# Performance work log

Hardware: AMD Instinct MI355X
Metric: run time of the kernel (lower is better)

## Reference

```python
import jax, jax.numpy as jnp
import numpy as np

B, N, D = 4, 4096, 512      # batch, seq_len, model width
DIM_K = 64                   # per-head key dim used ONLY for the 1/sqrt scale
PROJ = 512                   # dim_k*heads = dim_v*heads = 64*8


def setup_inputs() -> dict:
    key = jax.random.key(0)
    ks = jax.random.split(key, 11)
    glorot = lambda k, shape: jax.random.uniform(
        k, shape, jnp.float32,
        -np.sqrt(6.0 / (shape[0] + shape[1])), np.sqrt(6.0 / (shape[0] + shape[1])))
    return {
        "q": jax.random.normal(ks[0], (B, N, D), jnp.float32),
        "k": jax.random.normal(ks[1], (B, N, D), jnp.float32),
        "v": jax.random.normal(ks[2], (B, N, D), jnp.float32),
        "w_q": glorot(ks[3], (D, PROJ)),
        "w_k": glorot(ks[4], (D, PROJ)),
        "w_v": glorot(ks[5], (D, PROJ)),
        "w_mha": glorot(ks[6], (PROJ, D)),
        "b_q": jnp.zeros((1, 1, PROJ), jnp.float32),
        "b_k": jnp.zeros((1, 1, PROJ), jnp.float32),
        "b_v": jnp.zeros((1, 1, PROJ), jnp.float32),
        "b_mha": jnp.zeros((1, 1, D), jnp.float32),
    }


def reference(q, k, v, w_q, w_k, w_v, w_mha, b_q, b_k, b_v, b_mha):
    # Projections (tensordot over last axis + broadcast bias)
    qp = jnp.einsum('bnd,de->bne', q, w_q) + b_q
    kp = jnp.einsum('bnd,de->bne', k, w_k) + b_k
    vp = jnp.einsum('bnd,de->bne', v, w_v) + b_v
    # NOTE: original call() forgets to pass heads=self.heads, so heads=1:
    # a single attention over the full PROJ width, scaled by sqrt(DIM_K).
    atts = jnp.einsum('bqe,bke->bqk', qp, kp) / np.sqrt(DIM_K).astype(np.float32)
    atts = jax.nn.softmax(atts, axis=-1)      # [B, N, N]
    dpa = jnp.einsum('bqk,bke->bqe', atts, vp)
    return jnp.einsum('bne,ed->bnd', dpa, w_mha) + b_mha
```

## Files before the change

### kernel.cpp

```cpp
#include <hip/hip_runtime.h>
#include <hip/hip_bf16.h>


typedef __attribute__((ext_vector_type(8))) short bf16x8;
typedef __attribute__((ext_vector_type(4))) float f32x4;

#define NB 4
#define NN 4096
#define ND 512

__device__ __forceinline__ f32x4 mfma16(bf16x8 a, bf16x8 b, f32x4 c) {
    return __builtin_amdgcn_mfma_f32_16x16x32_bf16(a, b, c, 0, 0, 0);
}
__device__ __forceinline__ short f2bf(float f) {
    __hip_bfloat16 h = __float2bfloat16(f);
    return *reinterpret_cast<short*>(&h);
}

typedef __attribute__((address_space(1))) const unsigned int gls_gt;
typedef __attribute__((address_space(3))) unsigned int gls_lt;
__device__ __forceinline__ void gll16(const void* g, void* l) {
    __builtin_amdgcn_global_load_lds((gls_gt*)g, (gls_lt*)l, 16, 0, 0);
}

#define DPP_ROR_STEP(V, CTRL, OP)                                              \
    {                                                                          \
        int _t = __builtin_amdgcn_update_dpp(0, __float_as_int(V), (CTRL),     \
                                             0xf, 0xf, true);                  \
        (V) = OP((V), __int_as_float(_t));                                     \
    }
__device__ __forceinline__ float faddf(float a, float b) { return a + b; }
__device__ __forceinline__ float rmax16(float v) {
    DPP_ROR_STEP(v, 0x128, fmaxf)
    DPP_ROR_STEP(v, 0x124, fmaxf)
    DPP_ROR_STEP(v, 0x122, fmaxf)
    DPP_ROR_STEP(v, 0x121, fmaxf)
    return v;
}
__device__ __forceinline__ float rsum16(float v) {
    DPP_ROR_STEP(v, 0x128, faddf)
    DPP_ROR_STEP(v, 0x124, faddf)
    DPP_ROR_STEP(v, 0x122, faddf)
    DPP_ROR_STEP(v, 0x121, faddf)
    return v;
}

struct Ptrs4 {
    const float* in[4];
    short* out[4];
};

__global__ void transpose_w(Ptrs4 p) {
    __shared__ short tile[32][33];
    const float* in = p.in[blockIdx.z];
    short* out = p.out[blockIdx.z];
    int r0 = blockIdx.y * 32, c0 = blockIdx.x * 32;
    int tx = threadIdx.x, ty = threadIdx.y;
    for (int i = 0; i < 32; i += 8)
        tile[ty + i][tx] = f2bf(in[(r0 + ty + i) * 512 + c0 + tx]);
    __syncthreads();
    for (int i = 0; i < 32; i += 8)
        out[(c0 + ty + i) * 512 + r0 + tx] = tile[tx][ty + i];
}

template <int AF32, int VT, int OF32>
__global__ __launch_bounds__(256, 2) void gemm_bt_bias(
    const void* __restrict__ Av, const short* __restrict__ Bt,
    const float* __restrict__ bias, void* __restrict__ C) {
    __shared__ __align__(1024) char As[2][16384];
    __shared__ __align__(1024) char Bs[2][16384];
    int tid = threadIdx.x;
    int lane = tid & 63, w = tid >> 6;
    int l15 = lane & 15, l4 = lane >> 4;
    int wr2 = (w & 1) * 64, wc2 = (w >> 1) * 64;
    int m0 = blockIdx.x * 128, n0 = blockIdx.y * 128;
    f32x4 acc[16] = {};

    int sr = lane >> 3;
    int sd = ((lane & 7) ^ sr) << 3;

#define STAGE_B(BUF, KT)                                                    \
    {                                                                       \
        _Pragma("unroll")                                                   \
        for (int i = 0; i < 4; i++) {                                       \
            int rbase = i * 32 + w * 8;                                     \
            gll16(&Bt[(size_t)(n0 + rbase + sr) * 512 + (KT) + sd],         \
                  Bs[BUF] + rbase * 128);                                   \
        }                                                                   \
    }
#define STAGE_A16(BUF, KT)                                                  \
    {                                                                       \
        const short* A16 = (const short*)Av;                                \
        _Pragma("unroll")                                                   \
        for (int i = 0; i < 4; i++) {                                       \
            int rbase = i * 32 + w * 8;                                     \
            gll16(&A16[(size_t)(m0 + rbase + sr) * 512 + (KT) + sd],        \
                  As[BUF] + rbase * 128);                                   \
        }                                                                   \
    }

    float4 areg[8];
    int arow = w * 32 + (lane >> 4);
    int akc = lane & 15;
#define LOAD_A32(KT)                                                        \
    {                                                                       \
        const float* A32 = (const float*)Av;                                \
        _Pragma("unroll")                                                   \
        for (int inst = 0; inst < 8; inst++)                                \
            areg[inst] = ((const float4*)(A32 +                             \
                (size_t)(m0 + arow + inst * 4) * 512 + (KT)))[akc];         \
    }
#define WRITE_A32(BUF)                                                      \
    {                                                                       \
        _Pragma("unroll")                                                   \
        for (int inst = 0; inst < 8; inst++) {                              \
            int r = arow + inst * 4;                                        \
            short pk[4];                                                    \
            pk[0] = f2bf(areg[inst].x); pk[1] = f2bf(areg[inst].y);         \
            pk[2] = f2bf(areg[inst].z); pk[3] = f2bf(areg[inst].w);         \
            *(long long*)(As[BUF] + r * 128 +                               \
                (((akc >> 1) ^ (r & 7)) << 4) + ((akc & 1) << 3)) =         \
                *(const long long*)pk;                                      \
        }                                                                   \
    }

    if (AF32) {
        LOAD_A32(0);
        STAGE_B(0, 0);
        WRITE_A32(0);
    } else {
        STAGE_A16(0, 0);
        STAGE_B(0, 0);
    }
    for (int t = 0; t < 8; t++) {
        __syncthreads();
        if (t < 7) {
            if (AF32) {
                LOAD_A32((t + 1) * 64);
            } else {
                STAGE_A16((t + 1) & 1, (t + 1) * 64);
            }
            STAGE_B((t + 1) & 1, (t + 1) * 64);
        }
        const char* Ab = As[t & 1];
        const char* Bb = Bs[t & 1];
#pragma unroll
        for (int kb = 0; kb < 2; kb++) {
            int ph = ((((kb << 2) | l4) ^ (l15 & 7)) << 4);
            bf16x8 af[4], bfr[4];
#pragma unroll
            for (int mi = 0; mi < 4; mi++)
                af[mi] = *(const bf16x8*)(Ab + (wr2 + mi * 16 + l15) * 128 + ph);
#pragma unroll
            for (int ni = 0; ni < 4; ni++)
                bfr[ni] = *(const bf16x8*)(Bb + (wc2 + ni * 16 + l15) * 128 + ph);
#pragma unroll
            for (int mi = 0; mi < 4; mi++)
#pragma unroll
                for (int ni = 0; ni < 4; ni++)
                    acc[mi * 4 + ni] = mfma16(af[mi], bfr[ni], acc[mi * 4 + ni]);
        }
        if (AF32 && t < 7) WRITE_A32((t + 1) & 1);
    }
#undef STAGE_B
#undef STAGE_A16
#undef LOAD_A32
#undef WRITE_A32
    if (OF32) {
        for (int mi = 0; mi < 4; mi++)
            for (int ni = 0; ni < 4; ni++) {
                f32x4 vv = acc[mi * 4 + ni];
                int col = n0 + wc2 + ni * 16 + l15;
                float bv = bias[col];
                for (int r = 0; r < 4; r++) {
                    int row = m0 + wr2 + mi * 16 + l4 * 4 + r;
                    ((float*)C)[(size_t)row * 512 + col] = vv[r] + bv;
                }
            }
    } else if (VT) {
        __syncthreads();
        short* Ct = (short*)As;
#pragma unroll
        for (int mi = 0; mi < 4; mi++)
#pragma unroll
            for (int ni = 0; ni < 4; ni++) {
                f32x4 vv = acc[mi * 4 + ni];
                int col = wc2 + ni * 16 + l15;
                float bv = bias[n0 + col];
                int r0w = wr2 + mi * 16 + l4 * 4;
                short pk[4];
#pragma unroll
                for (int r = 0; r < 4; r++) pk[r] = f2bf(vv[r] + bv);
                int byteoff = col * 256 + ((r0w * 2) ^ ((col & 7) << 4));
                *(long long*)((char*)Ct + byteoff) = *(const long long*)pk;
            }
        __syncthreads();
        int b = m0 >> 12;
        short* Cb = (short*)C + (size_t)b * (ND * NN) + (m0 & 4095);
#pragma unroll
        for (int s = 0; s < 8; s++) {
            int col = (tid >> 4) + 16 * s;
            int j = tid & 15;
            int byteoff = col * 256 + ((16 * j) ^ ((col & 7) << 4));
            bf16x8 vvv = *(const bf16x8*)((char*)Ct + byteoff);
            *(bf16x8*)(Cb + (size_t)(n0 + col) * NN + 8 * j) = vvv;
        }
    } else {
        __syncthreads();
        short* Ct = (short*)As;
#pragma unroll
        for (int mi = 0; mi < 4; mi++)
#pragma unroll
            for (int ni = 0; ni < 4; ni++) {
                f32x4 vv = acc[mi * 4 + ni];
                int col = wc2 + ni * 16 + l15;
                float bv = bias[n0 + col];
#pragma unroll
                for (int r = 0; r < 4; r++) {
                    int row = wr2 + mi * 16 + l4 * 4 + r;
                    int byteoff = row * 256 + ((col * 2) ^ ((row & 3) << 5));
                    *(short*)((char*)Ct + byteoff) = f2bf(vv[r] + bv);
                }
            }
        __syncthreads();
#pragma unroll
        for (int s = 0; s < 8; s++) {
            int row = (tid >> 4) + 16 * s;
            int j = tid & 15;
            int byteoff = row * 256 + ((16 * j) ^ ((row & 3) << 5));
            bf16x8 vvv = *(const bf16x8*)((char*)Ct + byteoff);
            *(bf16x8*)((short*)C + (size_t)(m0 + row) * 512 + n0 + 8 * j) = vvv;
        }
    }
}

__global__ __launch_bounds__(512, 2) void flash_attn(
    const short* __restrict__ qp, const short* __restrict__ kp,
    const short* __restrict__ vpT, short* __restrict__ dpa) {
    __shared__ __align__(1024) char KsB[65536];
    __shared__ __align__(1024) char VsB[65536];
    __shared__ __align__(16)   char PldB[8192];
    __shared__ float SexM[128];
    __shared__ float SexS[128];

    int tid = threadIdx.x;
    int lane = tid & 63, w = tid >> 6;
    int l15 = lane & 15, l4 = lane >> 4;
    int wr = w & 3;
    int wc = w >> 2;
    int b = blockIdx.y;
    int q0 = blockIdx.x * 64;

    const short* qpb = qp + b * (NN * ND);
    const short* kpb = kp + b * (NN * ND);
    const short* vtb = vpT + b * (ND * NN);

    bf16x8 qf[16];
    {
        const short* qrow = qpb + (q0 + wr * 16 + l15) * ND + l4 * 8;
#pragma unroll
        for (int kb = 0; kb < 16; kb++) qf[kb] = *(const bf16x8*)(qrow + kb * 32);
    }
    f32x4 oacc[16] = {};
    float m_run[4], l_run[4];
#pragma unroll
    for (int r = 0; r < 4; r++) { m_run[r] = -1e30f; l_run[r] = 0.f; }

    const int vsl0 = ((l4 ^ (l15 & 7)) << 4);
    const int vsl1 = vsl0 ^ 64;

#define STAGE_K(J0)                                                         \
    {                                                                       \
        _Pragma("unroll")                                                   \
        for (int c = 0; c < 8; c++) {                                       \
            int key = w * 8 + c;                                            \
            const short* src = kpb + (size_t)((J0) + key) * ND +            \
                               ((lane ^ (key & 15)) << 3);                  \
            gll16(src, KsB + key * 1024);                                   \
        }                                                                   \
    }
#define STAGE_V(J0)                                                         \
    {                                                                       \
        _Pragma("unroll")                                                   \
        for (int c = 0; c < 8; c++) {                                       \
            int g = w * 8 + c;                                              \
            int e = g * 8 + (lane >> 3);                                    \
            const short* src = vtb + (size_t)e * NN + (J0) +                \
                               (((lane & 7) ^ (e & 7)) << 3);               \
            gll16(src, VsB + g * 1024);                                     \
        }                                                                   \
    }

    STAGE_K(0);
    STAGE_V(0);
    __syncthreads();

    for (int j0 = 0; j0 < NN; j0 += 64) {
        f32x4 s0 = {}, s1 = {};
        {
            const char* kb0 = KsB + (32 * wc + l15) * 1024;
            const char* kb1 = kb0 + 16 * 1024;
#pragma unroll
            for (int kb = 0; kb < 16; kb++) {
                int sl = ((((kb << 2) | l4) ^ l15) << 4);
                s0 = mfma16(qf[kb], *(const bf16x8*)(kb0 + sl), s0);
                s1 = mfma16(qf[kb], *(const bf16x8*)(kb1 + sl), s1);
            }
        }
        float vv0[4], vv1[4], mx[4], ss[4], p0[4], p1[4];
#pragma unroll
        for (int r = 0; r < 4; r++) {
            vv0[r] = s0[r] * 0.125f;
            vv1[r] = s1[r] * 0.125f;
            mx[r] = rmax16(fmaxf(vv0[r], vv1[r]));
        }
#pragma unroll
        for (int r = 0; r < 4; r++) {
            p0[r] = __expf(vv0[r] - mx[r]);
            p1[r] = __expf(vv1[r] - mx[r]);
            ss[r] = rsum16(p0[r] + p1[r]);
        }
        int row4 = wr * 16 + l4 * 4;
        if (l15 == 0) {
#pragma unroll
            for (int r = 0; r < 4; r++) {
                SexM[wc * 64 + row4 + r] = mx[r];
                SexS[wc * 64 + row4 + r] = ss[r];
            }
        }
        __syncthreads();
        float al4[4];
#pragma unroll
        for (int r = 0; r < 4; r++) {
            int row = row4 + r;
            float mo = SexM[(wc ^ 1) * 64 + row];
            float so = SexS[(wc ^ 1) * 64 + row];
            float mt = fmaxf(mx[r], mo);
            float st = ss[r] * __expf(mx[r] - mt) + so * __expf(mo - mt);
            float mn = fmaxf(m_run[r], mt);
            float al = __expf(m_run[r] - mn);
            l_run[r] = l_run[r] * al + st * __expf(mt - mn);
            m_run[r] = mn;
            al4[r] = al;
            float fs = __expf(mx[r] - mn);
            int rw7 = row & 7;
            char* prow = PldB + row * 128;
            int col0 = wc * 32 + l15;
            *(short*)(prow + (((col0 >> 3) ^ rw7) << 4) + ((col0 & 7) << 1)) = f2bf(p0[r] * fs);
            int col1 = col0 + 16;
            *(short*)(prow + (((col1 >> 3) ^ rw7) << 4) + ((col1 & 7) << 1)) = f2bf(p1[r] * fs);
        }
        {
            bool need = (al4[0] != 1.f) | (al4[1] != 1.f) |
                        (al4[2] != 1.f) | (al4[3] != 1.f);
            if (__any(need)) {
#pragma unroll
                for (int t = 0; t < 16; t++)
#pragma unroll
                    for (int r = 0; r < 4; r++) oacc[t][r] *= al4[r];
            }
        }
        __syncthreads();
        if (j0 + 64 < NN) STAGE_K(j0 + 64);
        bf16x8 pa0, pa1;
        {
            const char* prow = PldB + (wr * 16 + l15) * 128;
            pa0 = *(const bf16x8*)(prow + vsl0);
            pa1 = *(const bf16x8*)(prow + vsl1);
        }
#pragma unroll
        for (int eh = 0; eh < 2; eh++) {
#pragma unroll
            for (int i = 0; i < 8; i++) {
                const char* vb = VsB + (eh * 256 + 32 * i + 16 * wc + l15) * 128;
                int oi = eh * 8 + i;
                oacc[oi] = mfma16(pa0, *(const bf16x8*)(vb + vsl0), oacc[oi]);
                oacc[oi] = mfma16(pa1, *(const bf16x8*)(vb + vsl1), oacc[oi]);
            }
        }
        __syncthreads();
        if (j0 + 64 < NN) STAGE_V(j0 + 64);
    }
    float li[4];
#pragma unroll
    for (int r = 0; r < 4; r++) li[r] = 1.f / l_run[r];
    short* dpb = dpa + b * (NN * ND);
#pragma unroll
    for (int eh = 0; eh < 2; eh++)
#pragma unroll
        for (int i = 0; i < 8; i++) {
            int col = (16 * eh + 2 * i + wc) * 16 + l15;
#pragma unroll
            for (int r = 0; r < 4; r++) {
                int row = q0 + wr * 16 + l4 * 4 + r;
                dpb[row * ND + col] = f2bf(oacc[eh * 8 + i][r] * li[r]);
            }
        }
}

extern "C" void kernel_launch(void* const* d_in, const int* in_sizes, int n_in,
                              void* d_out, int out_size, void* d_ws, size_t ws_size,
                              hipStream_t stream) {
    const float* q     = (const float*)d_in[0];
    const float* k     = (const float*)d_in[1];
    const float* v     = (const float*)d_in[2];
    const float* w_q   = (const float*)d_in[3];
    const float* w_k   = (const float*)d_in[4];
    const float* w_v   = (const float*)d_in[5];
    const float* w_mha = (const float*)d_in[6];
    const float* b_q   = (const float*)d_in[7];
    const float* b_k   = (const float*)d_in[8];
    const float* b_v   = (const float*)d_in[9];
    const float* b_mha = (const float*)d_in[10];

    const size_t T = (size_t)NB * NN * ND;
    short* ws  = (short*)d_ws;
    short* qp  = ws;
    short* kp  = qp + T;
    short* vpT = kp + T;
    short* dpa = vpT + T;
    short* Wt  = dpa + T;

    Ptrs4 p;
    p.in[0] = w_q;   p.out[0] = Wt;
    p.in[1] = w_k;   p.out[1] = Wt + 262144;
    p.in[2] = w_v;   p.out[2] = Wt + 524288;
    p.in[3] = w_mha; p.out[3] = Wt + 786432;
    transpose_w<<<dim3(16, 16, 4), dim3(32, 8), 0, stream>>>(p);

    gemm_bt_bias<1, 0, 0><<<dim3(128, 4), 256, 0, stream>>>(q, Wt,          b_q, qp);
    gemm_bt_bias<1, 0, 0><<<dim3(128, 4), 256, 0, stream>>>(k, Wt + 262144, b_k, kp);
    gemm_bt_bias<1, 1, 0><<<dim3(128, 4), 256, 0, stream>>>(v, Wt + 524288, b_v, vpT);

    flash_attn<<<dim3(64, 4), 512, 0, stream>>>(qp, kp, vpT, dpa);

    gemm_bt_bias<0, 0, 1><<<dim3(128, 4), 256, 0, stream>>>(dpa, Wt + 786432, b_mha, d_out);
}
```

Baseline: 462.7 us.

## Software-pipeline flash attention with 32-key tiles and double-buffered K

Shrinks the key tile from 64 to 32 and double-buffers K in shared memory so the QK^T and softmax-statistics step for the next tile is computed before the barrier, overlapping with the PV MMA of the current tile. It also replaces one full __syncthreads with a custom lgkmcnt-wait barrier, and shared memory per block drops from about 138KB to about 102KB. The tradeoff is twice as many iterations and barriers, smaller MFMA batches per sync, and a more delicate buffer ordering that needs correct barrier placement.

```diff
diff --git a/kernel.cpp b/kernel.cpp
--- a/kernel.cpp
+++ b/kernel.cpp
@@ -21,6 +21,13 @@
 typedef __attribute__((address_space(3))) unsigned int gls_lt;
 __device__ __forceinline__ void gll16(const void* g, void* l) {
     __builtin_amdgcn_global_load_lds((gls_gt*)g, (gls_lt*)l, 16, 0, 0);
+}
+
+__device__ __forceinline__ void barrier_lgkm0() {
+    asm volatile("s_waitcnt lgkmcnt(0)" ::: "memory");
+    __builtin_amdgcn_s_barrier();
+    asm volatile("" ::: "memory");
+    __builtin_amdgcn_sched_barrier(0);
 }
 
 #define DPP_ROR_STEP(V, CTRL, OP)                                              \
@@ -237,9 +244,9 @@
 __global__ __launch_bounds__(512, 2) void flash_attn(
     const short* __restrict__ qp, const short* __restrict__ kp,
     const short* __restrict__ vpT, short* __restrict__ dpa) {
-    __shared__ __align__(1024) char KsB[65536];
-    __shared__ __align__(1024) char VsB[65536];
-    __shared__ __align__(16)   char PldB[8192];
+    __shared__ __align__(1024) char KsB[2][32768];
+    __shared__ __align__(1024) char VsB[32768];
+    __shared__ __align__(16)   char PldB[4096];
     __shared__ float SexM[128];
     __shared__ float SexS[128];
 
@@ -266,69 +273,68 @@
 #pragma unroll
     for (int r = 0; r < 4; r++) { m_run[r] = -1e30f; l_run[r] = 0.f; }
 
-    const int vsl0 = ((l4 ^ (l15 & 7)) << 4);
-    const int vsl1 = vsl0 ^ 64;
-
-#define STAGE_K(J0)                                                         \
-    {                                                                       \
-        _Pragma("unroll")                                                   \
-        for (int c = 0; c < 8; c++) {                                       \
-            int key = w * 8 + c;                                            \
+    float mx[4], ss[4], p0[4];
+
+#define STAGE_K(DST, J0)                                                    \
+    {                                                                       \
+        _Pragma("unroll")                                                   \
+        for (int c = 0; c < 4; c++) {                                       \
+            int key = w * 4 + c;                                            \
             const short* src = kpb + (size_t)((J0) + key) * ND +            \
                                ((lane ^ (key & 15)) << 3);                  \
-            gll16(src, KsB + key * 1024);                                   \
+            gll16(src, (DST) + key * 1024);                                 \
         }                                                                   \
     }
 #define STAGE_V(J0)                                                         \
     {                                                                       \
         _Pragma("unroll")                                                   \
-        for (int c = 0; c < 8; c++) {                                       \
-            int g = w * 8 + c;                                              \
-            int e = g * 8 + (lane >> 3);                                    \
-            const short* src = vtb + (size_t)e * NN + (J0) +                \
-                               (((lane & 7) ^ (e & 7)) << 3);               \
+        for (int c = 0; c < 4; c++) {                                       \
+            int g = w * 4 + c;                                              \
+            int e = g * 16 + (lane >> 2);                                   \
+            int d = (lane & 3) ^ ((e >> 1) & 3);                            \
+            const short* src = vtb + (size_t)e * NN + (J0) + (d << 3);      \
             gll16(src, VsB + g * 1024);                                     \
         }                                                                   \
     }
-
-    STAGE_K(0);
+#define QKT_STATS(KBUF)                                                     \
+    {                                                                       \
+        f32x4 s0 = {};                                                      \
+        const char* kb0 = (KBUF) + (16 * wc + l15) * 1024;                  \
+        _Pragma("unroll")                                                   \
+        for (int kb = 0; kb < 16; kb++) {                                   \
+            int sl = ((((kb << 2) | l4) ^ l15) << 4);                       \
+            s0 = mfma16(qf[kb], *(const bf16x8*)(kb0 + sl), s0);            \
+        }                                                                   \
+        float vvs[4];                                                       \
+        _Pragma("unroll")                                                   \
+        for (int r = 0; r < 4; r++) {                                       \
+            vvs[r] = s0[r] * 0.125f;                                        \
+            mx[r] = rmax16(vvs[r]);                                         \
+        }                                                                   \
+        _Pragma("unroll")                                                   \
+        for (int r = 0; r < 4; r++) {                                       \
+            p0[r] = __expf(vvs[r] - mx[r]);                                 \
+            ss[r] = rsum16(p0[r]);                                          \
+        }                                                                   \
+        int row4q = wr * 16 + l4 * 4;                                       \
+        if (l15 == 0) {                                                     \
+            _Pragma("unroll")                                               \
+            for (int r = 0; r < 4; r++) {                                   \
+                SexM[wc * 64 + row4q + r] = mx[r];                          \
+                SexS[wc * 64 + row4q + r] = ss[r];                          \
+            }                                                               \
+        }                                                                   \
+    }
+
+    STAGE_K(KsB[0], 0);
     STAGE_V(0);
     __syncthreads();
-
-    for (int j0 = 0; j0 < NN; j0 += 64) {
-        f32x4 s0 = {}, s1 = {};
-        {
-            const char* kb0 = KsB + (32 * wc + l15) * 1024;
-            const char* kb1 = kb0 + 16 * 1024;
-#pragma unroll
-            for (int kb = 0; kb < 16; kb++) {
-                int sl = ((((kb << 2) | l4) ^ l15) << 4);
-                s0 = mfma16(qf[kb], *(const bf16x8*)(kb0 + sl), s0);
-                s1 = mfma16(qf[kb], *(const bf16x8*)(kb1 + sl), s1);
-            }
-        }
-        float vv0[4], vv1[4], mx[4], ss[4], p0[4], p1[4];
-#pragma unroll
-        for (int r = 0; r < 4; r++) {
-            vv0[r] = s0[r] * 0.125f;
-            vv1[r] = s1[r] * 0.125f;
-            mx[r] = rmax16(fmaxf(vv0[r], vv1[r]));
-        }
-#pragma unroll
-        for (int r = 0; r < 4; r++) {
-            p0[r] = __expf(vv0[r] - mx[r]);
-            p1[r] = __expf(vv1[r] - mx[r]);
-            ss[r] = rsum16(p0[r] + p1[r]);
-        }
+    QKT_STATS(KsB[0]);
+    STAGE_K(KsB[1], 32);
+    barrier_lgkm0();
+
+    for (int t = 0; t < 128; t++) {
         int row4 = wr * 16 + l4 * 4;
-        if (l15 == 0) {
-#pragma unroll
-            for (int r = 0; r < 4; r++) {
-                SexM[wc * 64 + row4 + r] = mx[r];
-                SexS[wc * 64 + row4 + r] = ss[r];
-            }
-        }
-        __syncthreads();
         float al4[4];
 #pragma unroll
         for (int r = 0; r < 4; r++) {
@@ -343,59 +349,51 @@
             m_run[r] = mn;
             al4[r] = al;
             float fs = __expf(mx[r] - mn);
-            int rw7 = row & 7;
-            char* prow = PldB + row * 128;
-            int col0 = wc * 32 + l15;
-            *(short*)(prow + (((col0 >> 3) ^ rw7) << 4) + ((col0 & 7) << 1)) = f2bf(p0[r] * fs);
-            int col1 = col0 + 16;
-            *(short*)(prow + (((col1 >> 3) ^ rw7) << 4) + ((col1 & 7) << 1)) = f2bf(p1[r] * fs);
+            int c0 = wc * 16 + l15;
+            *(short*)(PldB + row * 64 + (((c0 >> 3) ^ ((row >> 1) & 3)) << 4) +
+                      ((c0 & 7) << 1)) = f2bf(p0[r] * fs);
         }
         {
             bool need = (al4[0] != 1.f) | (al4[1] != 1.f) |
                         (al4[2] != 1.f) | (al4[3] != 1.f);
             if (__any(need)) {
 #pragma unroll
-                for (int t = 0; t < 16; t++)
-#pragma unroll
-                    for (int r = 0; r < 4; r++) oacc[t][r] *= al4[r];
-            }
-        }
-        __syncthreads();
-        if (j0 + 64 < NN) STAGE_K(j0 + 64);
-        bf16x8 pa0, pa1;
+                for (int i = 0; i < 16; i++)
+#pragma unroll
+                    for (int r = 0; r < 4; r++) oacc[i][r] *= al4[r];
+            }
+        }
+        __syncthreads();
+        if (t < 126) STAGE_K(KsB[t & 1], (t + 2) * 32);
         {
-            const char* prow = PldB + (wr * 16 + l15) * 128;
-            pa0 = *(const bf16x8*)(prow + vsl0);
-            pa1 = *(const bf16x8*)(prow + vsl1);
-        }
-#pragma unroll
-        for (int eh = 0; eh < 2; eh++) {
-#pragma unroll
-            for (int i = 0; i < 8; i++) {
-                const char* vb = VsB + (eh * 256 + 32 * i + 16 * wc + l15) * 128;
-                int oi = eh * 8 + i;
-                oacc[oi] = mfma16(pa0, *(const bf16x8*)(vb + vsl0), oacc[oi]);
-                oacc[oi] = mfma16(pa1, *(const bf16x8*)(vb + vsl1), oacc[oi]);
-            }
-        }
-        __syncthreads();
-        if (j0 + 64 < NN) STAGE_V(j0 + 64);
+            int prow = wr * 16 + l15;
+            bf16x8 pa = *(const bf16x8*)(
+                PldB + prow * 64 + ((l4 ^ ((prow >> 1) & 3)) << 4));
+#pragma unroll
+            for (int i = 0; i < 16; i++) {
+                int e = (2 * i + wc) * 16 + l15;
+                const bf16x8* vb = (const bf16x8*)(
+                    VsB + e * 64 + ((l4 ^ ((e >> 1) & 3)) << 4));
+                oacc[i] = mfma16(pa, *vb, oacc[i]);
+            }
+        }
+        if (t < 127) QKT_STATS(KsB[(t + 1) & 1]);
+        barrier_lgkm0();
+        if (t < 127) STAGE_V((t + 1) * 32);
     }
     float li[4];
 #pragma unroll
     for (int r = 0; r < 4; r++) li[r] = 1.f / l_run[r];
     short* dpb = dpa + b * (NN * ND);
 #pragma unroll
-    for (int eh = 0; eh < 2; eh++)
-#pragma unroll
-        for (int i = 0; i < 8; i++) {
-            int col = (16 * eh + 2 * i + wc) * 16 + l15;
-#pragma unroll
-            for (int r = 0; r < 4; r++) {
-                int row = q0 + wr * 16 + l4 * 4 + r;
-                dpb[row * ND + col] = f2bf(oacc[eh * 8 + i][r] * li[r]);
-            }
-        }
+    for (int i = 0; i < 16; i++) {
+        int col = (2 * i + wc) * 16 + l15;
+#pragma unroll
+        for (int r = 0; r < 4; r++) {
+            int row = q0 + wr * 16 + l4 * 4 + r;
+            dpb[row * ND + col] = f2bf(oacc[i][r] * li[r]);
+        }
+    }
 }
 
 extern "C" void kernel_launch(void* const* d_in, const int* in_sizes, int n_in,
```

Measured after the change: 535.1 us. 1.16x slower.

## Remap PV output tiles so each wave owns a 64x64 block of output columns

Applied to the files above, without the earlier changes.

The P·V stage is re-tiled so each of the 8 waves computes all 64 query rows for its own 64-column slice of the value dimension, instead of 16 rows by 256 interleaved columns. Each wave then loads 8 P fragments and 8 V fragments into registers and reuses them across a 4x4 grid of MFMAs, which cuts redundant LDS reads of V. Rescale factors and final row sums now go through shared arrays, and the K prefetch plus a barrier move earlier so the rescale can read them. The cost is an extra barrier per iteration and more register pressure from holding 16 fragments.

```diff
diff --git a/kernel.cpp b/kernel.cpp
--- a/kernel.cpp
+++ b/kernel.cpp
@@ -242,12 +242,15 @@
     __shared__ __align__(16)   char PldB[8192];
     __shared__ float SexM[128];
     __shared__ float SexS[128];
+    __shared__ float arow[64];
+    __shared__ float lrowF[64];
 
     int tid = threadIdx.x;
     int lane = tid & 63, w = tid >> 6;
     int l15 = lane & 15, l4 = lane >> 4;
     int wr = w & 3;
     int wc = w >> 2;
+    int e0 = w * 64;
     int b = blockIdx.y;
     int q0 = blockIdx.x * 64;
 
@@ -265,9 +268,6 @@
     float m_run[4], l_run[4];
 #pragma unroll
     for (int r = 0; r < 4; r++) { m_run[r] = -1e30f; l_run[r] = 0.f; }
-
-    const int vsl0 = ((l4 ^ (l15 & 7)) << 4);
-    const int vsl1 = vsl0 ^ 64;
 
 #define STAGE_K(J0)                                                         \
     {                                                                       \
@@ -329,7 +329,6 @@
             }
         }
         __syncthreads();
-        float al4[4];
 #pragma unroll
         for (int r = 0; r < 4; r++) {
             int row = row4 + r;
@@ -341,8 +340,8 @@
             float al = __expf(m_run[r] - mn);
             l_run[r] = l_run[r] * al + st * __expf(mt - mn);
             m_run[r] = mn;
-            al4[r] = al;
             float fs = __expf(mx[r] - mn);
+            if (wc == 0 && l15 == 0) arow[row] = al;
             int rw7 = row & 7;
             char* prow = PldB + row * 128;
             int col0 = wc * 32 + l15;
@@ -350,52 +349,79 @@
             int col1 = col0 + 16;
             *(short*)(prow + (((col1 >> 3) ^ rw7) << 4) + ((col1 & 7) << 1)) = f2bf(p1[r] * fs);
         }
+        __syncthreads();
+        if (j0 + 64 < NN) STAGE_K(j0 + 64);
         {
-            bool need = (al4[0] != 1.f) | (al4[1] != 1.f) |
-                        (al4[2] != 1.f) | (al4[3] != 1.f);
+            float alq[4][4];
+            bool need = false;
+#pragma unroll
+            for (int qt = 0; qt < 4; qt++)
+#pragma unroll
+                for (int r = 0; r < 4; r++) {
+                    alq[qt][r] = arow[qt * 16 + l4 * 4 + r];
+                    need |= (alq[qt][r] != 1.0f);
+                }
             if (__any(need)) {
 #pragma unroll
-                for (int t = 0; t < 16; t++)
-#pragma unroll
-                    for (int r = 0; r < 4; r++) oacc[t][r] *= al4[r];
-            }
-        }
-        __syncthreads();
-        if (j0 + 64 < NN) STAGE_K(j0 + 64);
-        bf16x8 pa0, pa1;
+                for (int qt = 0; qt < 4; qt++)
+#pragma unroll
+                    for (int et = 0; et < 4; et++)
+#pragma unroll
+                        for (int r = 0; r < 4; r++)
+                            oacc[qt * 4 + et][r] *= alq[qt][r];
+            }
+        }
+        bf16x8 pa[8];
+        bf16x8 vf[8];
         {
-            const char* prow = PldB + (wr * 16 + l15) * 128;
-            pa0 = *(const bf16x8*)(prow + vsl0);
-            pa1 = *(const bf16x8*)(prow + vsl1);
-        }
-#pragma unroll
-        for (int eh = 0; eh < 2; eh++) {
-#pragma unroll
-            for (int i = 0; i < 8; i++) {
-                const char* vb = VsB + (eh * 256 + 32 * i + 16 * wc + l15) * 128;
-                int oi = eh * 8 + i;
-                oacc[oi] = mfma16(pa0, *(const bf16x8*)(vb + vsl0), oacc[oi]);
-                oacc[oi] = mfma16(pa1, *(const bf16x8*)(vb + vsl1), oacc[oi]);
-            }
-        }
+            int sw = l15 & 7;
+#pragma unroll
+            for (int qt = 0; qt < 4; qt++) {
+                const char* prow = PldB + (qt * 16 + l15) * 128;
+#pragma unroll
+                for (int jb = 0; jb < 2; jb++)
+                    pa[qt * 2 + jb] = *(const bf16x8*)(prow + (((jb * 4 + l4) ^ sw) << 4));
+            }
+#pragma unroll
+            for (int et = 0; et < 4; et++) {
+                const char* vrow = VsB + (e0 + et * 16 + l15) * 128;
+#pragma unroll
+                for (int jb = 0; jb < 2; jb++)
+                    vf[et * 2 + jb] = *(const bf16x8*)(vrow + (((jb * 4 + l4) ^ sw) << 4));
+            }
+        }
+#pragma unroll
+        for (int qt = 0; qt < 4; qt++)
+#pragma unroll
+            for (int et = 0; et < 4; et++) {
+                int oi = qt * 4 + et;
+                oacc[oi] = mfma16(pa[qt * 2 + 0], vf[et * 2 + 0], oacc[oi]);
+                oacc[oi] = mfma16(pa[qt * 2 + 1], vf[et * 2 + 1], oacc[oi]);
+            }
         __syncthreads();
         if (j0 + 64 < NN) STAGE_V(j0 + 64);
     }
-    float li[4];
-#pragma unroll
-    for (int r = 0; r < 4; r++) li[r] = 1.f / l_run[r];
+    if (wc == 0 && l15 == 0) {
+#pragma unroll
+        for (int r = 0; r < 4; r++) lrowF[wr * 16 + l4 * 4 + r] = l_run[r];
+    }
+    __syncthreads();
     short* dpb = dpa + b * (NN * ND);
 #pragma unroll
-    for (int eh = 0; eh < 2; eh++)
-#pragma unroll
-        for (int i = 0; i < 8; i++) {
-            int col = (16 * eh + 2 * i + wc) * 16 + l15;
+    for (int qt = 0; qt < 4; qt++) {
+        float li[4];
+#pragma unroll
+        for (int r = 0; r < 4; r++) li[r] = 1.f / lrowF[qt * 16 + l4 * 4 + r];
+#pragma unroll
+        for (int et = 0; et < 4; et++) {
+            int col = e0 + et * 16 + l15;
 #pragma unroll
             for (int r = 0; r < 4; r++) {
-                int row = q0 + wr * 16 + l4 * 4 + r;
-                dpb[row * ND + col] = f2bf(oacc[eh * 8 + i][r] * li[r]);
-            }
-        }
+                int row = q0 + qt * 16 + l4 * 4 + r;
+                dpb[row * ND + col] = f2bf(oacc[qt * 4 + et][r] * li[r]);
+            }
+        }
+    }
 }
 
 extern "C" void kernel_launch(void* const* d_in, const int* in_sizes, int n_in,
```

After: 811.7 us. 1.75x slower.
